# Kernel optimization log

Measured on AMD Instinct MI355X. Metric: run time of the kernel, lower is better.

## Reference

```python
import jax, jax.numpy as jnp
import numpy as np

BETA = 4.0  # temperature of soft cluster assignment in filling loss


def _pairwise_sq_dist(a, b):
    # a: [N,D], b: [K,D] -> [N,K] squared euclidean distances
    return (jnp.sum(a * a, -1, keepdims=True)
            - 2.0 * (a @ b.T)
            + jnp.sum(b * b, -1)[None, :])


def setup_inputs() -> dict:
    key = jax.random.key(0)
    k1, k2, k3, k4 = jax.random.split(key, 4)
    N, D, K = 131072, 64, 16
    x = jax.random.normal(k1, (N, D), jnp.float32)
    cluster_centers = jax.random.normal(k2, (K, D), jnp.float32)
    target = jax.random.normal(k3, (N, D), jnp.float32)
    ft = jax.random.uniform(k4, (K,), jnp.float32)
    filling_target = ft / ft.sum()
    # prediction = kmeans assignment of the fixed target set (computed once, constant)
    prediction = jnp.argmin(_pairwise_sq_dist(target, cluster_centers), axis=-1)
    return {"x": x, "cluster_centers": cluster_centers,
            "filling_target": filling_target, "target": target,
            "prediction": prediction}


def reference(x, cluster_centers, filling_target, target, prediction):
    N, D = x.shape
    Nt = target.shape[0]
    K = cluster_centers.shape[0]
    BIG = jnp.finfo(x.dtype).max  # padding value that sorts to the end

    d2 = _pairwise_sq_dist(x, cluster_centers)  # [N,K]

    # --- cluster filling MSE: soft assignment fractions vs filling_target ---
    soft = jax.nn.softmax(-BETA * d2, axis=-1)          # [N,K]
    filling = soft.mean(axis=0)                          # [K]
    loss_fil = jnp.mean((filling - filling_target) ** 2)

    # --- per-cluster sorted (per-dimension 1D) Wasserstein distance ---
    pred_x = jax.lax.stop_gradient(jnp.argmin(d2, axis=-1))  # kmeans_predict(x).detach()
    L = min(N, Nt)  # static upper bound on per-cluster min_size
    rows = jnp.arange(L)

    loss_med = jnp.zeros((), x.dtype)
    for k in range(K):  # fixed structural loop over clusters
        mx = pred_x == k
        mt = prediction == k
        m = jnp.minimum(mx.sum(), mt.sum())  # min_size (dynamic value, static shapes)
        # keep only the FIRST m members (original order), as x[in_cluster][:m]
        keep_x = mx & ((jnp.cumsum(mx) - 1) < m)
        keep_t = mt & ((jnp.cumsum(mt) - 1) < m)
        # mask out non-members with BIG so they sort to the bottom, sort per dim
        xs = jnp.sort(jnp.where(keep_x[:, None], x, BIG), axis=0)[:L]       # [L,D]
        ts = jnp.sort(jnp.where(keep_t[:, None], target, BIG), axis=0)[:L]  # [L,D]
        valid = (rows < m)[:, None]                                          # [L,1]
        diff = jnp.where(valid, jnp.abs(xs - ts), 0.0)
        # mean(|sort(x) - sort(y)|) over the m x D selected elements
        denom = (m * D).astype(x.dtype)
        loss_med = loss_med + jnp.where(m > 0, diff.sum() / denom, 0.0)

    return loss_fil + loss_med
```

## Files before the change

### kernel.cpp

```cpp
#include <hip/hip_runtime.h>
#include <stdint.h>

#define N_ROWS 131072
#define DIMS 64
#define KCL 16
#define BETA 4.0f
#define NBLK 512
#define CHUNK 16384
#define STH 1024
#define SEG_STRIDE 263168
#define VOFF (1u<<21)

typedef unsigned long long u64;
typedef unsigned int u32;

__device__ __forceinline__ u32 enc_f(float f) {
  u32 u = __float_as_uint(f);
  return (u & 0x80000000u) ? ~u : (u | 0x80000000u);
}
__device__ __forceinline__ float dec_f(u32 e) {
  u32 u = (e & 0x80000000u) ? (e & 0x7FFFFFFFu) : ~e;
  return __uint_as_float(u);
}
__device__ __forceinline__ u32 U4(u32 u) { return u ^ ((u >> 3) & 7u); }

#define CS(a,b,dd) { u32 _mn = min(a,b), _mx = max(a,b); a = (dd)?_mn:_mx; b = (dd)?_mx:_mn; }
#define CSV(A,B,D) { CS(A.x,B.x,D) CS(A.y,B.y,D) CS(A.z,B.z,D) CS(A.w,B.w,D) }

#define M16G(a,b,c,d,e,f,g,h,i2,j2,k2,l,m,n,o,p,D) \
  CS(a,i2,D) CS(b,j2,D) CS(c,k2,D) CS(d,l,D) CS(e,m,D) CS(f,n,D) CS(g,o,D) CS(h,p,D) \
  CS(a,e,D)  CS(b,f,D)  CS(c,g,D)  CS(d,h,D) CS(i2,m,D) CS(j2,n,D) CS(k2,o,D) CS(l,p,D) \
  CS(a,c,D)  CS(b,d,D)  CS(e,g,D)  CS(f,h,D) CS(i2,k2,D) CS(j2,l,D) CS(m,o,D) CS(n,p,D) \
  CS(a,b,D)  CS(c,d,D)  CS(e,f,D)  CS(g,h,D) CS(i2,j2,D) CS(k2,l,D) CS(m,n,D) CS(o,p,D)

#define SORT16G(a,b,c,d,e,f,g,h,i2,j2,k2,l,m,n,o,p,D) \
  CS(a,b,D) CS(c,d,!(D)) CS(e,f,D) CS(g,h,!(D)) CS(i2,j2,D) CS(k2,l,!(D)) CS(m,n,D) CS(o,p,!(D)) \
  CS(a,c,D) CS(b,d,D) CS(e,g,!(D)) CS(f,h,!(D)) CS(i2,k2,D) CS(j2,l,D) CS(m,o,!(D)) CS(n,p,!(D)) \
  CS(a,b,D) CS(c,d,D) CS(e,f,!(D)) CS(g,h,!(D)) CS(i2,j2,D) CS(k2,l,D) CS(m,n,!(D)) CS(o,p,!(D)) \
  CS(a,e,D) CS(b,f,D) CS(c,g,D) CS(d,h,D) CS(i2,m,!(D)) CS(j2,n,!(D)) CS(k2,o,!(D)) CS(l,p,!(D)) \
  CS(a,c,D) CS(b,d,D) CS(e,g,D) CS(f,h,D) CS(i2,k2,!(D)) CS(j2,l,!(D)) CS(m,o,!(D)) CS(n,p,!(D)) \
  CS(a,b,D) CS(c,d,D) CS(e,f,D) CS(g,h,D) CS(i2,j2,!(D)) CS(k2,l,!(D)) CS(m,n,!(D)) CS(o,p,!(D)) \
  M16G(a,b,c,d,e,f,g,h,i2,j2,k2,l,m,n,o,p,D)

#define MERGE16F(D) M16G(r0,r1,r2,r3,r4,r5,r6,r7,r8,r9,r10,r11,r12,r13,r14,r15,D)
#define SORT16F(D)  SORT16G(r0,r1,r2,r3,r4,r5,r6,r7,r8,r9,r10,r11,r12,r13,r14,r15,D)

#define LOADTILE16(src) \
  { uint4 _a0=src[U4(ub+0)],_a1=src[U4(ub+1)],_a2=src[U4(ub+2)],_a3=src[U4(ub+3)]; \
    r0=_a0.x;r1=_a0.y;r2=_a0.z;r3=_a0.w; r4=_a1.x;r5=_a1.y;r6=_a1.z;r7=_a1.w; \
    r8=_a2.x;r9=_a2.y;r10=_a2.z;r11=_a2.w; r12=_a3.x;r13=_a3.y;r14=_a3.z;r15=_a3.w; }

#define STORETILE16(dst) \
  { dst[U4(ub+0)]=make_uint4(r0,r1,r2,r3);   dst[U4(ub+1)]=make_uint4(r4,r5,r6,r7); \
    dst[U4(ub+2)]=make_uint4(r8,r9,r10,r11); dst[U4(ub+3)]=make_uint4(r12,r13,r14,r15); }

__device__ __forceinline__ void wave_tail(uint4* lds4, u32 RU, u32 Lw, u32 gbase,
                                          u32 k, u32 jtop, u32 lane)
{
  u32 j = jtop;
  while (j >= 32u) {
    u32 ud = j >> 3;
    if (lane < (Lw >> 4)) {
      u32 bu = RU + (((lane & ~(ud - 1u)) << 2) | (lane & (ud - 1u)));
      bool up = (((gbase + (bu << 2)) & k) == 0u);
      uint4 A0 = lds4[U4(bu)],           A1 = lds4[U4(bu + ud)],
            A2 = lds4[U4(bu + 2u * ud)], A3 = lds4[U4(bu + 3u * ud)];
      CSV(A0,A2,up) CSV(A1,A3,up)
      CSV(A0,A1,up) CSV(A2,A3,up)
      lds4[U4(bu)] = A0;           lds4[U4(bu + ud)] = A1;
      lds4[U4(bu + 2u * ud)] = A2; lds4[U4(bu + 3u * ud)] = A3;
    }
    j >>= 2;
  }
  if (j == 16u) {
    u32 total = Lw >> 3;
    for (u32 inst = lane; inst < total; inst += 64u) {
      u32 bu = RU + (((inst & ~3u) << 1) | (inst & 3u));
      bool up = (((gbase + (bu << 2)) & k) == 0u);
      uint4 A = lds4[U4(bu)], B = lds4[U4(bu + 4u)];
      CSV(A,B,up)
      lds4[U4(bu)] = A; lds4[U4(bu + 4u)] = B;
    }
  }
}

__device__ __forceinline__ void cross1(uint4* lds4, u32 Wn, u32 gb, u32 k, u32 jtop, u32 tid)
{
  u32 ud = jtop >> 2;
  u32 total = Wn >> 3;
  for (u32 inst = tid; inst < total; inst += STH) {
    u32 bu = ((inst & ~(ud - 1u)) << 1) | (inst & (ud - 1u));
    bool up = (((gb + (bu << 2)) & k) == 0u);
    uint4 A = lds4[U4(bu)], B = lds4[U4(bu + ud)];
    CSV(A,B,up)
    lds4[U4(bu)] = A; lds4[U4(bu + ud)] = B;
  }
}
__device__ __forceinline__ void cross2(uint4* lds4, u32 Wn, u32 gb, u32 k, u32 jtop, u32 tid)
{
  u32 ud = jtop >> 3;
  u32 total = Wn >> 4;
  for (u32 inst = tid; inst < total; inst += STH) {
    u32 bu = ((inst & ~(ud - 1u)) << 2) | (inst & (ud - 1u));
    bool up = (((gb + (bu << 2)) & k) == 0u);
    uint4 A0 = lds4[U4(bu)],            A1 = lds4[U4(bu + ud)],
          A2 = lds4[U4(bu + 2u * ud)],  A3 = lds4[U4(bu + 3u * ud)];
    CSV(A0,A2,up) CSV(A1,A3,up)
    CSV(A0,A1,up) CSV(A2,A3,up)
    lds4[U4(bu)] = A0;           lds4[U4(bu + ud)] = A1;
    lds4[U4(bu + 2u * ud)] = A2; lds4[U4(bu + 3u * ud)] = A3;
  }
}
__device__ __forceinline__ void cross3(uint4* lds4, u32 Wn, u32 gb, u32 k, u32 jtop, u32 tid)
{
  u32 ud = jtop >> 4;
  u32 total = Wn >> 5;
  for (u32 inst = tid; inst < total; inst += STH) {
    u32 bu = ((inst & ~(ud - 1u)) << 3) | (inst & (ud - 1u));
    bool up = (((gb + (bu << 2)) & k) == 0u);
    uint4 A0 = lds4[U4(bu)],            A1 = lds4[U4(bu + ud)],
          A2 = lds4[U4(bu + 2u * ud)],  A3 = lds4[U4(bu + 3u * ud)],
          A4 = lds4[U4(bu + 4u * ud)],  A5 = lds4[U4(bu + 5u * ud)],
          A6 = lds4[U4(bu + 6u * ud)],  A7 = lds4[U4(bu + 7u * ud)];
    CSV(A0,A4,up) CSV(A1,A5,up) CSV(A2,A6,up) CSV(A3,A7,up)
    CSV(A0,A2,up) CSV(A1,A3,up) CSV(A4,A6,up) CSV(A5,A7,up)
    CSV(A0,A1,up) CSV(A2,A3,up) CSV(A4,A5,up) CSV(A6,A7,up)
    lds4[U4(bu)] = A0;           lds4[U4(bu + ud)] = A1;
    lds4[U4(bu + 2u * ud)] = A2; lds4[U4(bu + 3u * ud)] = A3;
    lds4[U4(bu + 4u * ud)] = A4; lds4[U4(bu + 5u * ud)] = A5;
    lds4[U4(bu + 6u * ud)] = A6; lds4[U4(bu + 7u * ud)] = A7;
  }
}

__global__ __launch_bounds__(256) void k_assign(
    const float* __restrict__ x, const float* __restrict__ centers,
    const int* __restrict__ predT, int* __restrict__ predX,
    float* __restrict__ fill_sum, u32* __restrict__ histX, u32* __restrict__ histT)
{
  __shared__ float c[KCL][DIMS];
  __shared__ float cn[KCL];
  __shared__ float fs[KCL];
  __shared__ u32 hx[KCL], ht[KCL];
  int tid = threadIdx.x;
  for (int t = tid; t < KCL * DIMS; t += 256) c[t / DIMS][t % DIMS] = centers[t];
  if (tid < KCL) { fs[tid] = 0.f; hx[tid] = 0; ht[tid] = 0; }
  __syncthreads();
  if (tid < KCL) {
    float s = 0.f;
    for (int d = 0; d < DIMS; ++d) s += c[tid][d] * c[tid][d];
    cn[tid] = s;
  }
  __syncthreads();
  int i = blockIdx.x * 256 + tid;
  const float4* xr = (const float4*)(x + (size_t)i * DIMS);
  float dot[KCL];
#pragma unroll
  for (int k = 0; k < KCL; ++k) dot[k] = 0.f;
  for (int t = 0; t < DIMS / 4; ++t) {
    float4 v = xr[t];
#pragma unroll
    for (int k = 0; k < KCL; ++k)
      dot[k] += v.x * c[k][4 * t] + v.y * c[k][4 * t + 1] + v.z * c[k][4 * t + 2] + v.w * c[k][4 * t + 3];
  }
  float sc[KCL];
  float smin = 3.0e38f; int kmin = 0;
#pragma unroll
  for (int k = 0; k < KCL; ++k) {
    sc[k] = cn[k] - 2.f * dot[k];
    if (sc[k] < smin) { smin = sc[k]; kmin = k; }
  }
  float e[KCL]; float esum = 0.f;
#pragma unroll
  for (int k = 0; k < KCL; ++k) { e[k] = expf(-BETA * (sc[k] - smin)); esum += e[k]; }
  float inv = 1.f / esum;
#pragma unroll
  for (int k = 0; k < KCL; ++k) atomicAdd(&fs[k], e[k] * inv);
  predX[i] = kmin;
  atomicAdd(&hx[kmin], 1u);
  atomicAdd(&ht[predT[i]], 1u);
  __syncthreads();
  if (tid < KCL) {
    histX[blockIdx.x * KCL + tid] = hx[tid];
    histT[blockIdx.x * KCL + tid] = ht[tid];
    atomicAdd(&fill_sum[tid], fs[tid]);
  }
}

__global__ __launch_bounds__(512) void k_scan(
    const u32* __restrict__ histX, const u32* __restrict__ histT,
    u32* __restrict__ baseX, u32* __restrict__ baseT,
    const float* __restrict__ fill_sum, const float* __restrict__ ftarget,
    int* __restrict__ m_out, float* __restrict__ w_out,
    int* __restrict__ p_out, int* __restrict__ pOff_out, int* __restrict__ mOff_out,
    int* __restrict__ nlo_out, float* __restrict__ loss_fil)
{
  __shared__ u32 part[2][KCL][17];
  __shared__ u32 tot[2][KCL];
  __shared__ float sq[KCL];
  __shared__ int sp[KCL];
  __shared__ int smv[KCL];
  int tid = threadIdx.x;
  int side = tid >> 8;
  int rem = tid & 255;
  int c = rem >> 4;
  int sub = rem & 15;
  const u32* hist = side ? histT : histX;
  u32* base = side ? baseT : baseX;
  int b0 = sub * 32;
  u32 s = 0;
  for (int b = b0; b < b0 + 32; ++b) s += hist[b * KCL + c];
  part[side][c][sub] = s;
  __syncthreads();
  if (sub == 0) {
    u32 run = 0;
    for (int t = 0; t < 16; ++t) { u32 v = part[side][c][t]; part[side][c][t] = run; run += v; }
    tot[side][c] = run;
  }
  __syncthreads();
  u32 run = part[side][c][sub];
  for (int b = b0; b < b0 + 32; ++b) { base[b * KCL + c] = run; run += hist[b * KCL + c]; }
  if (tid < KCL) {
    int m = min((int)tot[0][tid], (int)tot[1][tid]);
    m_out[tid] = m;
    smv[tid] = m;
    w_out[tid] = (m > 0) ? 1.f / ((float)m * (float)DIMS) : 0.f;
    int pp = 32;
    while (pp < m) pp <<= 1;
    sp[tid] = pp;
    p_out[tid] = pp;
    int nlo = 0;
    if (pp > CHUNK) {
      int nch = pp / CHUNK;
      for (int j = 1; j < nch; j += 2) {
        int v = m - j * CHUNK;
        if (v < 0) v = 0;
        if (v > CHUNK) v = CHUNK;
        nlo += CHUNK - v;
      }
    }
    nlo_out[tid] = nlo;
    float d = fill_sum[tid] / (float)N_ROWS - ftarget[tid];
    sq[tid] = d * d;
  }
  __syncthreads();
  if (tid == 0) {
    float s2 = 0.f;
    int acc = 0, macc = 0;
    for (int k = 0; k < KCL; ++k) {
      s2 += sq[k];
      pOff_out[k] = acc;
      acc += sp[k];
      mOff_out[k] = macc;
      macc += smv[k];
    }
    pOff_out[KCL] = acc;
    mOff_out[KCL] = macc;
    *loss_fil = s2 / (float)KCL;
  }
}

__global__ __launch_bounds__(256) void k_rank(
    const int* __restrict__ predX, const int* __restrict__ predT,
    const u32* __restrict__ baseX, const u32* __restrict__ baseT,
    const int* __restrict__ mG, const int* __restrict__ mOffG,
    int* __restrict__ idxX, int* __restrict__ idxT)
{
  __shared__ int wcX[4][KCL], wcT[4][KCL];
  __shared__ int smo[KCL], sm2[KCL];
  int tid = threadIdx.x;
  int lane = tid & 63, wave = tid >> 6;
  if (tid < KCL) { smo[tid] = mOffG[tid]; sm2[tid] = mG[tid]; }
  int i = blockIdx.x * 256 + tid;
  int kx = predX[i], kt = predT[i];
  u64 below = (1ull << lane) - 1ull;
  int lrX = 0, lrT = 0;
  for (int cc = 0; cc < KCL; ++cc) {
    u64 mx = __ballot(kx == cc);
    u64 mt = __ballot(kt == cc);
    if (kx == cc) lrX = __popcll(mx & below);
    if (kt == cc) lrT = __popcll(mt & below);
    if (lane == 0) { wcX[wave][cc] = __popcll(mx); wcT[wave][cc] = __popcll(mt); }
  }
  __syncthreads();
  int wbX = 0, wbT = 0;
  for (int w2 = 0; w2 < wave; ++w2) { wbX += wcX[w2][kx]; wbT += wcT[w2][kt]; }
  int rX = (int)baseX[blockIdx.x * KCL + kx] + wbX + lrX;
  int rT = (int)baseT[blockIdx.x * KCL + kt] + wbT + lrT;
  if (rX < sm2[kx]) idxX[smo[kx] + rX] = i;
  if (rT < sm2[kt]) idxT[smo[kt] + rT] = i;
}

__global__ __launch_bounds__(256) void k_gather(
    const float* __restrict__ x, const float* __restrict__ tgt,
    const int* __restrict__ idxX, const int* __restrict__ idxT,
    const int* __restrict__ pOffG, const int* __restrict__ mOffG,
    const int* __restrict__ mG, const int* __restrict__ pG,
    u32* __restrict__ valX, u32* __restrict__ valT, int d0, int Dbc)
{
  __shared__ int spOff[KCL + 1];
  __shared__ int smo[KCL], sm2[KCL], sp2[KCL];
  int tid = threadIdx.x;
  if (tid <= KCL) spOff[tid] = pOffG[tid];
  if (tid < KCL) { smo[tid] = mOffG[tid]; sm2[tid] = mG[tid]; sp2[tid] = pG[tid]; }
  __syncthreads();
  int pos = blockIdx.x * 256 + tid;
  if (pos >= spOff[KCL]) return;
  int c = 0;
#pragma unroll
  for (int cc = 1; cc < KCL; ++cc) c += (pos >= spOff[cc]) ? 1 : 0;
  int rel = pos - spOff[c];
  u32* dx = valX + pos;
  u32* dt = valT + pos;
  if (rel < sm2[c]) {
    int w = smo[c] + rel;
    int iX = idxX[w], iT = idxT[w];
    if ((Dbc & 3) == 0) {
      const float4* xr = (const float4*)(x + (size_t)iX * DIMS + d0);
      const float4* tr = (const float4*)(tgt + (size_t)iT * DIMS + d0);
      for (int q = 0; q < (Dbc >> 2); ++q) {
        float4 a = xr[q];
        float4 b = tr[q];
        size_t base = (size_t)(4 * q) * SEG_STRIDE;
        dx[base]                  = enc_f(a.x);
        dx[base + SEG_STRIDE]     = enc_f(a.y);
        dx[base + 2 * (size_t)SEG_STRIDE] = enc_f(a.z);
        dx[base + 3 * (size_t)SEG_STRIDE] = enc_f(a.w);
        dt[base]                  = enc_f(b.x);
        dt[base + SEG_STRIDE]     = enc_f(b.y);
        dt[base + 2 * (size_t)SEG_STRIDE] = enc_f(b.z);
        dt[base + 3 * (size_t)SEG_STRIDE] = enc_f(b.w);
      }
    } else {
      const float* xr = x + (size_t)iX * DIMS + d0;
      const float* tr = tgt + (size_t)iT * DIMS + d0;
      for (int d = 0; d < Dbc; ++d) {
        dx[(size_t)d * SEG_STRIDE] = enc_f(xr[d]);
        dt[(size_t)d * SEG_STRIDE] = enc_f(tr[d]);
      }
    }
  } else {
    u32 pv = (sp2[c] > CHUNK && ((rel >> 14) & 1)) ? 0u : 0xFFFFFFFFu;
    for (int d = 0; d < Dbc; ++d) {
      dx[(size_t)d * SEG_STRIDE] = pv;
      dt[(size_t)d * SEG_STRIDE] = pv;
    }
  }
}

__global__ __launch_bounds__(STH, 8) void k_sort(
    u32* __restrict__ vbase, const int* __restrict__ pG, const int* __restrict__ pOffG,
    const int* __restrict__ mG)
{
  __shared__ __align__(16) u32 lds[CHUNK];
  uint4* lds4 = (uint4*)lds;
  int t = blockIdx.x, c = -1, sub = 0, acc = 0;
  for (int cc = 0; cc < KCL; ++cc) {
    int pc0 = pG[cc];
    int nc = (pc0 > CHUNK) ? (pc0 / CHUNK) : 1;
    if (t < acc + nc) { c = cc; sub = t - acc; break; }
    acc += nc;
  }
  if (c < 0) return;
  int pc = pG[c];
  u32 CH = (u32)min(pc, CHUNK);
  u32 gb = (u32)sub * (u32)CHUNK;
  int v = mG[c] - (int)gb;
  if (v > (int)CH) v = (int)CH;
  if (v <= 0) return;
  u32 W = 32u;
  while (W < (u32)v) W <<= 1;
  if (W > CH) W = CH;
  bool desc = (pc > CHUNK) && (sub & 1);
  u32 inv = desc ? 0xFFFFFFFFu : 0u;
  u32* seg = vbase + (size_t)blockIdx.y * SEG_STRIDE + pOffG[c] + gb;
  uint4* gp4 = (uint4*)seg;
  u32 tid = threadIdx.x;
  u32 lane = tid & 63u;
  u32 wv = tid >> 6;
  u32 ub = tid << 2;
  u32 bas = tid << 4;
  bool act = (bas < W);
  u32 RU = wv << 8;
  u32 runBase = wv << 10;
  bool wact = (runBase < W);
  u32 Lw = W - runBase; if (Lw > 1024u) Lw = 1024u;
  u32 r0,r1,r2,r3,r4,r5,r6,r7,r8,r9,r10,r11,r12,r13,r14,r15;

  if (act) {
    uint4 a0 = gp4[ub + 0], a1 = gp4[ub + 1], a2 = gp4[ub + 2], a3 = gp4[ub + 3];
    r0 = a0.x^inv; r1 = a0.y^inv; r2  = a0.z^inv; r3  = a0.w^inv;
    r4 = a1.x^inv; r5 = a1.y^inv; r6  = a1.z^inv; r7  = a1.w^inv;
    r8 = a2.x^inv; r9 = a2.y^inv; r10 = a2.z^inv; r11 = a2.w^inv;
    r12 = a3.x^inv; r13 = a3.y^inv; r14 = a3.z^inv; r15 = a3.w^inv;
    bool D = ((bas & 16u) == 0u);
    SORT16F(D);
    STORETILE16(lds4);
  }
  if (wact) {
    for (u32 k = 32u; k <= Lw; k <<= 1) {
      wave_tail(lds4, RU, Lw, 0u, k, k >> 1, lane);
      if (act) {
        LOADTILE16(lds4);
        bool D = ((bas & k) == 0u);
        MERGE16F(D);
        if (k < W) { STORETILE16(lds4); }
        else {
          gp4[ub + 0] = make_uint4(r0^inv, r1^inv, r2^inv, r3^inv);
          gp4[ub + 1] = make_uint4(r4^inv, r5^inv, r6^inv, r7^inv);
          gp4[ub + 2] = make_uint4(r8^inv, r9^inv, r10^inv, r11^inv);
          gp4[ub + 3] = make_uint4(r12^inv, r13^inv, r14^inv, r15^inv);
        }
      }
    }
  }

  if (W >= 2048u) {
    __syncthreads();
    for (u32 k = 2048u; k <= W; k <<= 1) {
      u32 jt = k >> 1;
      if (jt >= 8192u) {
        cross3(lds4, W, 0u, k, 8192u, tid);
        __syncthreads();
        cross1(lds4, W, 0u, k, 1024u, tid);
        __syncthreads();
      } else if (jt == 4096u) {
        cross3(lds4, W, 0u, k, 4096u, tid);
        __syncthreads();
      } else if (jt == 2048u) {
        cross2(lds4, W, 0u, k, 2048u, tid);
        __syncthreads();
      } else {
        cross1(lds4, W, 0u, k, 1024u, tid);
        __syncthreads();
      }
      if (wact) {
        wave_tail(lds4, RU, Lw, 0u, k, 512u, lane);
        if (act) {
          LOADTILE16(lds4);
          bool D = ((bas & k) == 0u);
          MERGE16F(D);
          if (k < W) { STORETILE16(lds4); }
          else {
            gp4[ub + 0] = make_uint4(r0^inv, r1^inv, r2^inv, r3^inv);
            gp4[ub + 1] = make_uint4(r4^inv, r5^inv, r6^inv, r7^inv);
            gp4[ub + 2] = make_uint4(r8^inv, r9^inv, r10^inv, r11^inv);
            gp4[ub + 3] = make_uint4(r12^inv, r13^inv, r14^inv, r15^inv);
          }
        }
      }
      if (k < W) __syncthreads();
    }
  }
}

__global__ __launch_bounds__(256) void k_gpass(
    u32* __restrict__ vbase, const int* __restrict__ pG, const int* __restrict__ pOffG,
    int kk, int j)
{
  u32* base = vbase + (size_t)blockIdx.y * SEG_STRIDE;
  int pb[KCL]; int tot = 0;
#pragma unroll
  for (int c = 0; c < KCL; ++c) {
    pb[c] = tot;
    int pc = pG[c];
    if (pc >= kk) tot += pc >> 1;
  }
  for (int g4 = (blockIdx.x * 256 + threadIdx.x) << 2; g4 < tot; g4 += gridDim.x * 256 * 4) {
    int c = 0;
#pragma unroll
    for (int cc = 1; cc < KCL; ++cc) c += (g4 >= pb[cc]) ? 1 : 0;
    int u = g4 - pb[c];
    int i = ((u & ~(j - 1)) << 1) | (u & (j - 1));
    bool up = ((i & kk) == 0);
    u32* s2 = base + pOffG[c];
    uint4 A = *(const uint4*)(s2 + i);
    uint4 B = *(const uint4*)(s2 + i + j);
    CS(A.x, B.x, up) CS(A.y, B.y, up) CS(A.z, B.z, up) CS(A.w, B.w, up)
    *(uint4*)(s2 + i) = A;
    *(uint4*)(s2 + i + j) = B;
  }
}

__global__ __launch_bounds__(STH, 8) void k_gfinish(
    u32* __restrict__ vbase, const int* __restrict__ pG, const int* __restrict__ pOffG, int kk)
{
  __shared__ __align__(16) u32 lds[CHUNK];
  uint4* lds4 = (uint4*)lds;
  int t = blockIdx.x, c = -1, sub = 0, acc = 0;
  for (int cc = 0; cc < KCL; ++cc) {
    int pc = pG[cc];
    if (pc < kk) continue;
    int nc = pc / CHUNK;
    if (t < acc + nc) { c = cc; sub = t - acc; break; }
    acc += nc;
  }
  if (c < 0) return;
  u32 gb = (u32)sub * (u32)CHUNK;
  u32* seg = vbase + (size_t)blockIdx.y * SEG_STRIDE + pOffG[c] + gb;
  uint4* gp4 = (uint4*)seg;
  u32 tid = threadIdx.x;
  u32 lane = tid & 63u;
  u32 wv = tid >> 6;
  u32 RU = wv << 8;
  u32 ub = tid << 2;
  u32 bas = tid << 4;
  u32 r0,r1,r2,r3,r4,r5,r6,r7,r8,r9,r10,r11,r12,r13,r14,r15;

  for (u32 uu = tid; uu < CHUNK / 4; uu += STH) lds4[U4(uu)] = gp4[uu];
  __syncthreads();
  cross3(lds4, (u32)CHUNK, gb, (u32)kk, 8192u, tid);
  __syncthreads();
  cross1(lds4, (u32)CHUNK, gb, (u32)kk, 1024u, tid);
  __syncthreads();
  wave_tail(lds4, RU, 1024u, gb, (u32)kk, 512u, lane);
  {
    LOADTILE16(lds4);
    bool up = (((gb + bas) & (u32)kk) == 0u);
    MERGE16F(up);
    gp4[ub + 0] = make_uint4(r0, r1, r2, r3);
    gp4[ub + 1] = make_uint4(r4, r5, r6, r7);
    gp4[ub + 2] = make_uint4(r8, r9, r10, r11);
    gp4[ub + 3] = make_uint4(r12, r13, r14, r15);
  }
}

__global__ __launch_bounds__(256) void k_reduce(
    const u32* __restrict__ valX, const u32* __restrict__ valT,
    const int* __restrict__ pOffG, const int* __restrict__ mOffG,
    const int* __restrict__ nloG,
    const float* __restrict__ wG, float* __restrict__ lossAcc)
{
  __shared__ int spOff[KCL];
  __shared__ int smo[KCL + 1];
  __shared__ int snlo[KCL];
  __shared__ float swt[KCL];
  __shared__ float red[256];
  int tid = threadIdx.x;
  if (tid <= KCL) smo[tid] = mOffG[tid];
  if (tid < KCL) { spOff[tid] = pOffG[tid]; snlo[tid] = nloG[tid]; swt[tid] = wG[tid]; }
  __syncthreads();
  int d = blockIdx.y;
  const u32* vx = valX + (size_t)d * SEG_STRIDE;
  const u32* vt = valT + (size_t)d * SEG_STRIDE;
  int M = smo[KCL];
  float s = 0.f;
  for (int w = blockIdx.x * 256 + tid; w < M; w += gridDim.x * 256) {
    int c = 0;
#pragma unroll
    for (int cc = 1; cc < KCL; ++cc) c += (w >= smo[cc]) ? 1 : 0;
    int pos = spOff[c] + snlo[c] + (w - smo[c]);
    float a = dec_f(vx[pos]), b = dec_f(vt[pos]);
    s += fabsf(a - b) * swt[c];
  }
  red[tid] = s;
  __syncthreads();
  for (int st = 128; st > 0; st >>= 1) {
    if (tid < st) red[tid] += red[tid + st];
    __syncthreads();
  }
  if (tid == 0) atomicAdd(lossAcc, red[0]);
}

__global__ void k_final(const float* __restrict__ lossAcc, const float* __restrict__ loss_fil,
                        float* __restrict__ out)
{
  out[0] = *lossAcc + *loss_fil;
}

extern "C" void kernel_launch(void* const* d_in, const int* in_sizes, int n_in,
                              void* d_out, int out_size, void* d_ws, size_t ws_size,
                              hipStream_t stream)
{
  const float* x       = (const float*)d_in[0];
  const float* centers = (const float*)d_in[1];
  const float* ftarget = (const float*)d_in[2];
  const float* tgt     = (const float*)d_in[3];
  const int*   predT   = (const int*)d_in[4];
  float* out = (float*)d_out;

  char* ws = (char*)d_ws;
  float* fill_sum = (float*)(ws + 0);
  float* lossAcc  = (float*)(ws + 64);
  float* loss_fil = (float*)(ws + 68);
  int*   m_buf    = (int*)(ws + 128);
  float* w_buf    = (float*)(ws + 192);
  int*   p_buf    = (int*)(ws + 256);
  int*   pOff     = (int*)(ws + 320);
  int*   mOff     = (int*)(ws + 400);
  u32* histX = (u32*)(ws + 512);
  u32* histT = (u32*)(ws + 512 + 32768);
  u32* baseX = (u32*)(ws + 512 + 65536);
  u32* baseT = (u32*)(ws + 512 + 98304);
  int* predX = (int*)(ws + 131584);
  int* idxX  = (int*)(ws + 655872);
  int* idxT  = (int*)(ws + 1180160);
  int* nlo_buf = (int*)(ws + 1704448);
  u32* vbase = (u32*)(ws + VOFF);

  size_t avail_elems = (ws_size > VOFF) ? ((ws_size - VOFF) / 4) : 0;
  int Db = (int)(avail_elems / (2ull * SEG_STRIDE));
  if (Db > DIMS) Db = DIMS;
  if (Db >= 4) Db &= ~3;
  if (Db < 1) Db = 1;

  hipMemsetAsync(ws, 0, 128, stream);
  k_assign<<<NBLK, 256, 0, stream>>>(x, centers, predT, predX, fill_sum, histX, histT);
  k_scan<<<1, 512, 0, stream>>>(histX, histT, baseX, baseT, fill_sum, ftarget,
                                m_buf, w_buf, p_buf, pOff, mOff, nlo_buf, loss_fil);
  k_rank<<<NBLK, 256, 0, stream>>>(predX, predT, baseX, baseT, m_buf, mOff, idxX, idxT);

  for (int d0 = 0; d0 < DIMS; d0 += Db) {
    int Dbc = (Db < DIMS - d0) ? Db : (DIMS - d0);
    u32* valX = vbase;
    u32* valT = vbase + (size_t)Dbc * SEG_STRIDE;
    k_gather<<<1028, 256, 0, stream>>>(x, tgt, idxX, idxT, pOff, mOff, m_buf, p_buf,
                                       valX, valT, d0, Dbc);
    k_sort<<<dim3(26, 2 * Dbc), STH, 0, stream>>>(vbase, p_buf, pOff, m_buf);
    for (int kk = 2 * CHUNK; kk <= N_ROWS; kk <<= 1) {
      for (int j = kk >> 1; j >= CHUNK; j >>= 1)
        k_gpass<<<dim3(16, 2 * Dbc), 256, 0, stream>>>(vbase, p_buf, pOff, kk, j);
      k_gfinish<<<dim3(16, 2 * Dbc), STH, 0, stream>>>(vbase, p_buf, pOff, kk);
    }
    k_reduce<<<dim3(32, Dbc), 256, 0, stream>>>(valX, valT, pOff, mOff, nlo_buf,
                                                w_buf, lossAcc);
  }
  k_final<<<1, 1, 0, stream>>>(lossAcc, loss_fil, out);
}
```

Before: 652.8 us.

## Use radix-8 wave bitonic steps, stage final stores through LDS, retune grids

The in-wave bitonic tail now handles three merge levels per LDS round trip with 8-element groups instead of two levels with 4, which cuts the number of LDS load/store passes. Final results are written back to LDS and then copied to global memory in a coalesced linear loop, instead of each thread storing its own scattered tile. Separately, the k_sort grid width grows, k_gpass uses fewer blocks for the larger merge stages, and the occupancy hint on k_gfinish is dropped. In exchange there is higher register pressure in the 8-way step and an extra barrier plus LDS pass before the write-out.

```diff
diff --git a/kernel.cpp b/kernel.cpp
--- a/kernel.cpp
+++ b/kernel.cpp
@@ -58,21 +58,38 @@
                                           u32 k, u32 jtop, u32 lane)
 {
   u32 j = jtop;
-  while (j >= 32u) {
-    u32 ud = j >> 3;
+  while (j >= 64u) {
+    u32 ju = j >> 4;
+    u32 ninst = Lw >> 5;
+    if (lane < ninst) {
+      u32 bu = RU + (((lane & ~(ju - 1u)) << 3) | (lane & (ju - 1u)));
+      bool up = (((gbase + (bu << 2)) & k) == 0u);
+      uint4 A0 = lds4[U4(bu)],            A1 = lds4[U4(bu + ju)],
+            A2 = lds4[U4(bu + 2u * ju)],  A3 = lds4[U4(bu + 3u * ju)],
+            A4 = lds4[U4(bu + 4u * ju)],  A5 = lds4[U4(bu + 5u * ju)],
+            A6 = lds4[U4(bu + 6u * ju)],  A7 = lds4[U4(bu + 7u * ju)];
+      CSV(A0,A4,up) CSV(A1,A5,up) CSV(A2,A6,up) CSV(A3,A7,up)
+      CSV(A0,A2,up) CSV(A1,A3,up) CSV(A4,A6,up) CSV(A5,A7,up)
+      CSV(A0,A1,up) CSV(A2,A3,up) CSV(A4,A5,up) CSV(A6,A7,up)
+      lds4[U4(bu)] = A0;           lds4[U4(bu + ju)] = A1;
+      lds4[U4(bu + 2u * ju)] = A2; lds4[U4(bu + 3u * ju)] = A3;
+      lds4[U4(bu + 4u * ju)] = A4; lds4[U4(bu + 5u * ju)] = A5;
+      lds4[U4(bu + 6u * ju)] = A6; lds4[U4(bu + 7u * ju)] = A7;
+    }
+    j >>= 3;
+  }
+  if (j == 32u) {
     if (lane < (Lw >> 4)) {
-      u32 bu = RU + (((lane & ~(ud - 1u)) << 2) | (lane & (ud - 1u)));
+      u32 bu = RU + (((lane & ~3u) << 2) | (lane & 3u));
       bool up = (((gbase + (bu << 2)) & k) == 0u);
-      uint4 A0 = lds4[U4(bu)],           A1 = lds4[U4(bu + ud)],
-            A2 = lds4[U4(bu + 2u * ud)], A3 = lds4[U4(bu + 3u * ud)];
+      uint4 A0 = lds4[U4(bu)],      A1 = lds4[U4(bu + 4u)],
+            A2 = lds4[U4(bu + 8u)], A3 = lds4[U4(bu + 12u)];
       CSV(A0,A2,up) CSV(A1,A3,up)
       CSV(A0,A1,up) CSV(A2,A3,up)
-      lds4[U4(bu)] = A0;           lds4[U4(bu + ud)] = A1;
-      lds4[U4(bu + 2u * ud)] = A2; lds4[U4(bu + 3u * ud)] = A3;
-    }
-    j >>= 2;
-  }
-  if (j == 16u) {
+      lds4[U4(bu)] = A0;      lds4[U4(bu + 4u)] = A1;
+      lds4[U4(bu + 8u)] = A2; lds4[U4(bu + 12u)] = A3;
+    }
+  } else if (j == 16u) {
     u32 total = Lw >> 3;
     for (u32 inst = lane; inst < total; inst += 64u) {
       u32 bu = RU + (((inst & ~3u) << 1) | (inst & 3u));
@@ -403,13 +420,7 @@
         LOADTILE16(lds4);
         bool D = ((bas & k) == 0u);
         MERGE16F(D);
-        if (k < W) { STORETILE16(lds4); }
-        else {
-          gp4[ub + 0] = make_uint4(r0^inv, r1^inv, r2^inv, r3^inv);
-          gp4[ub + 1] = make_uint4(r4^inv, r5^inv, r6^inv, r7^inv);
-          gp4[ub + 2] = make_uint4(r8^inv, r9^inv, r10^inv, r11^inv);
-          gp4[ub + 3] = make_uint4(r12^inv, r13^inv, r14^inv, r15^inv);
-        }
+        STORETILE16(lds4);
       }
     }
   }
@@ -434,23 +445,25 @@
         __syncthreads();
       }
       if (wact) {
-        wave_tail(lds4, RU, Lw, 0u, k, 512u, lane);
+        wave_tail(lds4, RU, Lw, 0u, k, 512u, tid & 63u);
         if (act) {
           LOADTILE16(lds4);
           bool D = ((bas & k) == 0u);
           MERGE16F(D);
-          if (k < W) { STORETILE16(lds4); }
-          else {
-            gp4[ub + 0] = make_uint4(r0^inv, r1^inv, r2^inv, r3^inv);
-            gp4[ub + 1] = make_uint4(r4^inv, r5^inv, r6^inv, r7^inv);
-            gp4[ub + 2] = make_uint4(r8^inv, r9^inv, r10^inv, r11^inv);
-            gp4[ub + 3] = make_uint4(r12^inv, r13^inv, r14^inv, r15^inv);
-          }
+          STORETILE16(lds4);
         }
       }
       if (k < W) __syncthreads();
     }
   }
+
+  __syncthreads();
+  for (u32 uu = tid; (uu << 2) < W; uu += STH) {
+    uint4 q = lds4[U4(uu)];
+    q.x ^= inv; q.y ^= inv; q.z ^= inv; q.w ^= inv;
+    gp4[uu] = q;
+  }
+  (void)lane;
 }
 
 __global__ __launch_bounds__(256) void k_gpass(
@@ -481,7 +494,7 @@
   }
 }
 
-__global__ __launch_bounds__(STH, 8) void k_gfinish(
+__global__ __launch_bounds__(STH) void k_gfinish(
     u32* __restrict__ vbase, const int* __restrict__ pG, const int* __restrict__ pOffG, int kk)
 {
   __shared__ __align__(16) u32 lds[CHUNK];
@@ -517,11 +530,10 @@
     LOADTILE16(lds4);
     bool up = (((gb + bas) & (u32)kk) == 0u);
     MERGE16F(up);
-    gp4[ub + 0] = make_uint4(r0, r1, r2, r3);
-    gp4[ub + 1] = make_uint4(r4, r5, r6, r7);
-    gp4[ub + 2] = make_uint4(r8, r9, r10, r11);
-    gp4[ub + 3] = make_uint4(r12, r13, r14, r15);
-  }
+    STORETILE16(lds4);
+  }
+  __syncthreads();
+  for (u32 uu = tid; uu < CHUNK / 4; uu += STH) gp4[uu] = lds4[U4(uu)];
 }
 
 __global__ __launch_bounds__(256) void k_reduce(
@@ -615,10 +627,11 @@
     u32* valT = vbase + (size_t)Dbc * SEG_STRIDE;
     k_gather<<<1028, 256, 0, stream>>>(x, tgt, idxX, idxT, pOff, mOff, m_buf, p_buf,
                                        valX, valT, d0, Dbc);
-    k_sort<<<dim3(26, 2 * Dbc), STH, 0, stream>>>(vbase, p_buf, pOff, m_buf);
+    k_sort<<<dim3(34, 2 * Dbc), STH, 0, stream>>>(vbase, p_buf, pOff, m_buf);
     for (int kk = 2 * CHUNK; kk <= N_ROWS; kk <<= 1) {
+      int gx = (kk == 2 * CHUNK) ? 16 : 8;
       for (int j = kk >> 1; j >= CHUNK; j >>= 1)
-        k_gpass<<<dim3(16, 2 * Dbc), 256, 0, stream>>>(vbase, p_buf, pOff, kk, j);
+        k_gpass<<<dim3(gx, 2 * Dbc), 256, 0, stream>>>(vbase, p_buf, pOff, kk, j);
       k_gfinish<<<dim3(16, 2 * Dbc), STH, 0, stream>>>(vbase, p_buf, pOff, kk);
     }
     k_reduce<<<dim3(32, Dbc), 256, 0, stream>>>(valX, valT, pOff, mOff, nlo_buf,
```

Result: slower. 805.8 us (+23.4%).
